# Kernel optimization log

Measured on AMD Instinct MI355X. Metric: run time of the kernel, lower is better.

The kernel has to match this reference:

```python
import jax, jax.numpy as jnp
import numpy as np

NUM_EXPERTS = 64
TOPK = 8
EPS = 1.1920929e-07  # torch.finfo(float32).eps


def setup_inputs() -> dict:
    key = jax.random.key(0)
    k1, k2 = jax.random.split(key)
    hidden_states = jax.random.normal(k1, (1, 4096, 4096), dtype=jnp.float32)
    wg_weight = jax.random.normal(k2, (NUM_EXPERTS, 4096), dtype=jnp.float32) * 0.02
    return {"hidden_states": hidden_states, "wg_weight": wg_weight}


def _routing(logits, capacity):
    # logits: [T, E]; capacity: static python int
    gates = jax.nn.softmax(logits, axis=1)                       # [T, E]
    _, idx = jax.lax.top_k(gates, TOPK)                          # [T, k]
    emask = jax.nn.one_hot(idx, NUM_EXPERTS, dtype=jnp.float32)  # [T, k, E]
    # sum of selected gate probs per token, clamped at fp32 eps
    gates_s = jnp.clip(jnp.einsum('tke,te->t', emask, gates), EPS)[:, None]
    router_probs = gates / gates_s                               # [T, E]
    # priority: cumulative position of each token within each expert,
    # scanned over (topk-major, token-minor) flattened order
    idx_flat = idx.T.reshape(-1)                                 # [k*T]
    mflat = jax.nn.one_hot(idx_flat, NUM_EXPERTS, dtype=jnp.int32)
    tp = jnp.cumsum(mflat, axis=0) * mflat - 1                   # [k*T, E]
    tp = tp.reshape(TOPK, -1, NUM_EXPERTS).transpose(1, 0, 2).max(axis=1)  # [T, E]
    valid = (tp >= 0) & (tp < capacity)                          # [T, E]
    tp = jnp.where(valid, tp, 0)
    dispatch_mask = jax.nn.one_hot(tp, capacity, dtype=jnp.bool_) & valid[:, :, None]  # [T, E, C]
    combine_weights = router_probs[:, :, None] * dispatch_mask   # [T, E, C]
    return combine_weights, dispatch_mask


def reference(hidden_states, wg_weight):
    b, s, h = hidden_states.shape
    x = hidden_states.reshape(-1, h).astype(jnp.float32)         # [T, H]
    logits = x @ wg_weight.T                                     # [T, E]
    # expert_capacity = max tokens assigned to any expert (data-dependent,
    # computed eagerly as in the torch .item() call)
    _, idx = jax.lax.top_k(jax.nn.softmax(logits, axis=1), TOPK)
    counts = jnp.bincount(idx.reshape(-1), length=NUM_EXPERTS)
    capacity = int(counts.max())
    return _routing(logits, capacity)
```

## Files before the change

### kernel.cpp

```cpp
#include <hip/hip_runtime.h>
#include <hip/hip_bf16.h>


#define TOK 4096
#define HID 4096
#define NE  64
#define NK  8

typedef double v4d __attribute__((ext_vector_type(4)));

__global__ __launch_bounds__(256) void gemm_logits_mfma(
    const float* __restrict__ x, const float* __restrict__ wg,
    double* __restrict__ partial, int kchunk, int* __restrict__ flag) {
  __shared__ float xs[64][68];
  __shared__ float wsh[64][68];
  const int tid  = threadIdx.x;
  const int lane = tid & 63;
  const int w    = tid >> 6;
  const int t0   = blockIdx.x * 64;
  const int k0   = blockIdx.y * kchunk;

  if (blockIdx.x == 0 && blockIdx.y == 0 && tid == 0) *flag = 0;

  v4d z = {0.0, 0.0, 0.0, 0.0};
  v4d pr = __builtin_amdgcn_mfma_f64_16x16x4f64((double)lane, 1.0, z, 0, 0, 0);
  v4d pc = __builtin_amdgcn_mfma_f64_16x16x4f64(1.0, (double)lane, z, 0, 0, 0);
  const int pv0 = (int)(pr[0] + 0.5);
  const int qv0 = (int)(pc[0] + 0.5);
  const bool a_kouter = ((pv0 & 3) == 0);
  const bool b_kouter = ((qv0 & 3) == 0);
  const int am = a_kouter ? (lane & 15) : (lane >> 2);
  const int ak = a_kouter ? (lane >> 4) : (lane & 3);
  const int bn = b_kouter ? (lane & 15) : (lane >> 2);
  const int bk = b_kouter ? (lane >> 4) : (lane & 3);
  int rmap[4], cmap[4];
#pragma unroll
  for (int v = 0; v < 4; ++v) {
    int V = (int)(pr[v] + 0.5);
    int rv = a_kouter ? ((V - 96) >> 2) : ((V - 6) >> 4);
    rmap[v] = rv < 0 ? 0 : (rv > 15 ? 15 : rv);
    int W = (int)(pc[v] + 0.5);
    int cv = b_kouter ? ((W - 96) >> 2) : ((W - 6) >> 4);
    cmap[v] = cv < 0 ? 0 : (cv > 15 ? 15 : cv);
  }

  v4d acc0 = {0.0, 0.0, 0.0, 0.0};
  v4d acc1 = acc0, acc2 = acc0, acc3 = acc0;

  const int lrow = tid >> 2;
  const int lcol = (tid & 3) * 16;

  for (int s = 0; s < kchunk; s += 64) {
    const int kk0 = k0 + s;
#pragma unroll
    for (int j = 0; j < 4; ++j) {
      *(float4*)&xs [lrow][lcol + j * 4] =
          *(const float4*)&x [(size_t)(t0 + lrow) * HID + kk0 + lcol + j * 4];
      *(float4*)&wsh[lrow][lcol + j * 4] =
          *(const float4*)&wg[(size_t)lrow * HID + kk0 + lcol + j * 4];
    }
    __syncthreads();
#pragma unroll
    for (int s4 = 0; s4 < 16; ++s4) {
      double a  = (double)xs [w * 16 + am][s4 * 4 + ak];
      double b0 = (double)wsh[ 0 + bn][s4 * 4 + bk];
      double b1 = (double)wsh[16 + bn][s4 * 4 + bk];
      double b2 = (double)wsh[32 + bn][s4 * 4 + bk];
      double b3 = (double)wsh[48 + bn][s4 * 4 + bk];
      acc0 = __builtin_amdgcn_mfma_f64_16x16x4f64(a, b0, acc0, 0, 0, 0);
      acc1 = __builtin_amdgcn_mfma_f64_16x16x4f64(a, b1, acc1, 0, 0, 0);
      acc2 = __builtin_amdgcn_mfma_f64_16x16x4f64(a, b2, acc2, 0, 0, 0);
      acc3 = __builtin_amdgcn_mfma_f64_16x16x4f64(a, b3, acc3, 0, 0, 0);
    }
    __syncthreads();
  }

  double* base = partial + (size_t)blockIdx.y * TOK * NE;
#pragma unroll
  for (int v = 0; v < 4; ++v) {
    const int row = t0 + w * 16 + rmap[v];
    const int col = cmap[v];
    double* rp = base + (size_t)row * NE;
    rp[ 0 + col] = acc0[v];
    rp[16 + col] = acc1[v];
    rp[32 + col] = acc2[v];
    rp[48 + col] = acc3[v];
  }
}

__global__ __launch_bounds__(256) void verify_kernel(
    const float* __restrict__ x, const float* __restrict__ wg,
    const double* __restrict__ partial, int nsplit, int* __restrict__ flag) {
  const int gid  = blockIdx.x * blockDim.x + threadIdx.x;
  const int wid  = gid >> 6;
  const int lane = gid & 63;
  const int t = (wid * 521) & (TOK - 1);
  const int e = wid & 63;
  double acc = 0.0;
  for (int k = lane; k < HID; k += 64)
    acc = fma((double)x[(size_t)t * HID + k], (double)wg[(size_t)e * HID + k], acc);
#pragma unroll
  for (int off = 32; off; off >>= 1) acc += __shfl_xor(acc, off);
  if (lane == 0) {
    double got = 0.0;
    for (int p = 0; p < nsplit; ++p)
      got += partial[(size_t)p * TOK * NE + (size_t)t * NE + e];
    if (!(fabs(got - acc) <= 1e-6)) atomicOr(flag, 1);
  }
}

__global__ __launch_bounds__(256) void repair_gemm(
    const float* __restrict__ x, const float* __restrict__ wg,
    double* __restrict__ partial, int nsplit, const int* __restrict__ flag) {
  if (*(volatile const int*)flag == 0) return;
  const int gid = blockIdx.x * 256 + threadIdx.x;
  const int t = gid >> 6;
  const int e = gid & 63;
  double acc = 0.0;
  for (int k = 0; k < HID; ++k)
    acc = fma((double)x[(size_t)t * HID + k], (double)wg[(size_t)e * HID + k], acc);
  partial[(size_t)t * NE + e] = acc;
  for (int p = 1; p < nsplit; ++p)
    partial[(size_t)p * TOK * NE + (size_t)t * NE + e] = 0.0;
}

__global__ __launch_bounds__(256) void topk_kernel(
    const double* __restrict__ partial, int nsplit,
    int* __restrict__ idx_kt, float* __restrict__ w_kt) {
  const int gid  = blockIdx.x * blockDim.x + threadIdx.x;
  const int t    = gid >> 6;
  const int lane = gid & 63;

  double v = 0.0;
  for (int p = 0; p < nsplit; ++p)
    v += partial[(size_t)p * TOK * NE + (size_t)t * NE + lane];

  double m = v;
#pragma unroll
  for (int off = 32; off; off >>= 1) {
    double o = __shfl_xor(m, off);
    m = o > m ? o : m;
  }
  double g = exp(v - m);
  double s = g;
#pragma unroll
  for (int off = 32; off; off >>= 1) s += __shfl_xor(s, off);
  double gate = g / s;

  float key = (float)gate;
  double ssel = 0.0;
  int my_k = -1;
#pragma unroll
  for (int k = 0; k < NK; ++k) {
    float bv = key;
    int   bi = lane;
#pragma unroll
    for (int off = 32; off; off >>= 1) {
      float ov = __shfl_xor(bv, off);
      int   oi = __shfl_xor(bi, off);
      if (ov > bv || (ov == bv && oi < bi)) { bv = ov; bi = oi; }
    }
    ssel += __shfl(gate, bi);
    if (lane == bi) { my_k = k; key = -1.0f; }
  }
  double gs = ssel;
  const double eps = (double)1.1920929e-07f;
  if (gs < eps) gs = eps;

  if (my_k >= 0) {
    idx_kt[my_k * TOK + t] = lane;
    w_kt [my_k * TOK + t] = (float)(gate / gs);
  }
}

__global__ __launch_bounds__(1024) void rank_kernel(
    const int* __restrict__ idx_kt, int* __restrict__ rank_kt) {
  const int e    = blockIdx.x;
  const int tid  = threadIdx.x;
  const int lane = tid & 63;
  const int w    = tid >> 6;
  __shared__ int wt[16];
  int running = 0;
  const unsigned long long below = (1ull << lane) - 1ull;

  for (int i0 = 0; i0 < NK * TOK; i0 += 1024) {
    const int i = i0 + tid;
    const bool mhit = (idx_kt[i] == e);
    unsigned long long mask = __ballot(mhit);
    if (lane == 0) wt[w] = __popcll(mask);
    __syncthreads();
    int woff = 0, tot = 0;
#pragma unroll
    for (int j = 0; j < 16; ++j) {
      int c = wt[j];
      tot += c;
      if (j < w) woff += c;
    }
    if (mhit) rank_kt[i] = running + woff + __popcll(mask & below);
    running += tot;
    __syncthreads();
  }
}

__global__ __launch_bounds__(256) void scatter_kernel(
    const int* __restrict__ idx_kt, const int* __restrict__ rank_kt,
    const float* __restrict__ w_kt, float* __restrict__ out, int C) {
  const int i = blockIdx.x * 256 + threadIdx.x;
  const int t = i & (TOK - 1);
  const int e = idx_kt[i];
  const int c = rank_kt[i];
  const float wv = w_kt[i];
  if (e >= 0 && e < NE && c >= 0 && c < C) {
    size_t off = ((size_t)t * NE + e) * (size_t)C + (size_t)c;
    out[off] = wv;
    out[(size_t)TOK * NE * C + off] = 1.0f;
  }
}

extern "C" void kernel_launch(void* const* d_in, const int* in_sizes, int n_in,
                              void* d_out, int out_size, void* d_ws, size_t ws_size,
                              hipStream_t stream) {
  const float* x  = (const float*)d_in[0];
  const float* wg = (const float*)d_in[1];
  float* out = (float*)d_out;

  const int C = out_size / (2 * TOK * NE);

  const size_t slab = (size_t)TOK * NE * sizeof(double);
  const size_t tail = 3 * (size_t)NK * TOK * sizeof(int);
  int nsplit = 8;
  while (nsplit > 1 && (size_t)nsplit * slab + tail + 64 > ws_size) nsplit >>= 1;
  const int kchunk = HID / nsplit;

  char* ws = (char*)d_ws;
  double* partial = (double*)ws;
  int*    idx_kt  = (int*)  (ws + (size_t)nsplit * slab);
  int*    rank_kt = (int*)  (ws + (size_t)nsplit * slab + (size_t)NK * TOK * 4);
  float*  w_kt    = (float*)(ws + (size_t)nsplit * slab + (size_t)NK * TOK * 8);
  int*    flag    = (int*)  (ws + (size_t)nsplit * slab + tail);

  hipMemsetAsync(d_out, 0, (size_t)out_size * sizeof(float), stream);

  dim3 ggrid(TOK / 64, nsplit);
  gemm_logits_mfma<<<ggrid, 256, 0, stream>>>(x, wg, partial, kchunk, flag);
  verify_kernel   <<<128, 256, 0, stream>>>(x, wg, partial, nsplit, flag);
  repair_gemm     <<<TOK * NE / 256, 256, 0, stream>>>(x, wg, partial, nsplit, flag);
  topk_kernel     <<<TOK * 64 / 256, 256, 0, stream>>>(partial, nsplit, idx_kt, w_kt);
  rank_kernel     <<<NE, 1024, 0, stream>>>(idx_kt, rank_kt);
  scatter_kernel  <<<NK * TOK / 256, 256, 0, stream>>>(idx_kt, rank_kt, w_kt, out, C);
}
```

Baseline: 1.264 ms.

## Fuse output zero-fill into logits GEMM and replace FP64 MFMA with FMA tiles

The separate hipMemsetAsync of the large dense output is removed. Extra blocks appended to the logits GEMM grid now zero the output with float4 stores, so the fill runs alongside the GEMM. The GEMM drops the FP64 MFMA path and its runtime lane-layout probing in favour of a scalar FP64 FMA register tile of 4x4 per thread. This removes the launch and serialization of the memset, but the FMA path may have lower throughput than MFMA, and it relies on out_size being a multiple of 4.

```diff
diff --git a/kernel.cpp b/kernel.cpp
--- a/kernel.cpp
+++ b/kernel.cpp
@@ -6,86 +6,88 @@
 #define HID 4096
 #define NE  64
 #define NK  8
-
-typedef double v4d __attribute__((ext_vector_type(4)));
-
-__global__ __launch_bounds__(256) void gemm_logits_mfma(
+#define FILLB 2048
+
+__global__ __launch_bounds__(256) void fused_gemm_fill(
     const float* __restrict__ x, const float* __restrict__ wg,
-    double* __restrict__ partial, int kchunk, int* __restrict__ flag) {
-  __shared__ float xs[64][68];
-  __shared__ float wsh[64][68];
-  const int tid  = threadIdx.x;
-  const int lane = tid & 63;
-  const int w    = tid >> 6;
-  const int t0   = blockIdx.x * 64;
-  const int k0   = blockIdx.y * kchunk;
-
-  if (blockIdx.x == 0 && blockIdx.y == 0 && tid == 0) *flag = 0;
-
-  v4d z = {0.0, 0.0, 0.0, 0.0};
-  v4d pr = __builtin_amdgcn_mfma_f64_16x16x4f64((double)lane, 1.0, z, 0, 0, 0);
-  v4d pc = __builtin_amdgcn_mfma_f64_16x16x4f64(1.0, (double)lane, z, 0, 0, 0);
-  const int pv0 = (int)(pr[0] + 0.5);
-  const int qv0 = (int)(pc[0] + 0.5);
-  const bool a_kouter = ((pv0 & 3) == 0);
-  const bool b_kouter = ((qv0 & 3) == 0);
-  const int am = a_kouter ? (lane & 15) : (lane >> 2);
-  const int ak = a_kouter ? (lane >> 4) : (lane & 3);
-  const int bn = b_kouter ? (lane & 15) : (lane >> 2);
-  const int bk = b_kouter ? (lane >> 4) : (lane & 3);
-  int rmap[4], cmap[4];
-#pragma unroll
-  for (int v = 0; v < 4; ++v) {
-    int V = (int)(pr[v] + 0.5);
-    int rv = a_kouter ? ((V - 96) >> 2) : ((V - 6) >> 4);
-    rmap[v] = rv < 0 ? 0 : (rv > 15 ? 15 : rv);
-    int W = (int)(pc[v] + 0.5);
-    int cv = b_kouter ? ((W - 96) >> 2) : ((W - 6) >> 4);
-    cmap[v] = cv < 0 ? 0 : (cv > 15 ? 15 : cv);
-  }
-
-  v4d acc0 = {0.0, 0.0, 0.0, 0.0};
-  v4d acc1 = acc0, acc2 = acc0, acc3 = acc0;
-
+    double* __restrict__ partial, int kchunk, int nsplit,
+    float* __restrict__ out, size_t n4, int* __restrict__ flag) {
+  __shared__ float xs [64][68];
+  __shared__ float wsf[64][65];
+  const int tid = threadIdx.x;
+  const int GB  = 64 * nsplit;
+
+  if ((int)blockIdx.x >= GB) {
+    const int fb = (int)blockIdx.x - GB;
+    const float4 z4 = make_float4(0.f, 0.f, 0.f, 0.f);
+    float4* o4 = (float4*)out;
+    for (size_t i = (size_t)fb * 256 + tid; i < n4; i += (size_t)FILLB * 256)
+      o4[i] = z4;
+    return;
+  }
+
+  if (blockIdx.x == 0 && tid == 0) *flag = 0;
+  const int bt   = (int)blockIdx.x & 63;
+  const int slab = (int)blockIdx.x >> 6;
+  const int t0 = bt * 64;
+  const int k0 = slab * kchunk;
+  const int te = tid & 15;
+  const int tt = tid >> 4;
   const int lrow = tid >> 2;
-  const int lcol = (tid & 3) * 16;
+  const int lc   = (tid & 3) * 16;
+
+  double acc[4][4];
+#pragma unroll
+  for (int i = 0; i < 4; ++i)
+#pragma unroll
+    for (int j = 0; j < 4; ++j) acc[i][j] = 0.0;
 
   for (int s = 0; s < kchunk; s += 64) {
-    const int kk0 = k0 + s;
+    const int kk = k0 + s;
 #pragma unroll
     for (int j = 0; j < 4; ++j) {
-      *(float4*)&xs [lrow][lcol + j * 4] =
-          *(const float4*)&x [(size_t)(t0 + lrow) * HID + kk0 + lcol + j * 4];
-      *(float4*)&wsh[lrow][lcol + j * 4] =
-          *(const float4*)&wg[(size_t)lrow * HID + kk0 + lcol + j * 4];
-    }
-    __syncthreads();
-#pragma unroll
-    for (int s4 = 0; s4 < 16; ++s4) {
-      double a  = (double)xs [w * 16 + am][s4 * 4 + ak];
-      double b0 = (double)wsh[ 0 + bn][s4 * 4 + bk];
-      double b1 = (double)wsh[16 + bn][s4 * 4 + bk];
-      double b2 = (double)wsh[32 + bn][s4 * 4 + bk];
-      double b3 = (double)wsh[48 + bn][s4 * 4 + bk];
-      acc0 = __builtin_amdgcn_mfma_f64_16x16x4f64(a, b0, acc0, 0, 0, 0);
-      acc1 = __builtin_amdgcn_mfma_f64_16x16x4f64(a, b1, acc1, 0, 0, 0);
-      acc2 = __builtin_amdgcn_mfma_f64_16x16x4f64(a, b2, acc2, 0, 0, 0);
-      acc3 = __builtin_amdgcn_mfma_f64_16x16x4f64(a, b3, acc3, 0, 0, 0);
-    }
-    __syncthreads();
-  }
-
-  double* base = partial + (size_t)blockIdx.y * TOK * NE;
-#pragma unroll
-  for (int v = 0; v < 4; ++v) {
-    const int row = t0 + w * 16 + rmap[v];
-    const int col = cmap[v];
-    double* rp = base + (size_t)row * NE;
-    rp[ 0 + col] = acc0[v];
-    rp[16 + col] = acc1[v];
-    rp[32 + col] = acc2[v];
-    rp[48 + col] = acc3[v];
-  }
+      float4 xv = *(const float4*)&x [(size_t)(t0 + lrow) * HID + kk + lc + 4 * j];
+      *(float4*)&xs[lrow][lc + 4 * j] = xv;
+      float4 wv = *(const float4*)&wg[(size_t)lrow * HID + kk + lc + 4 * j];
+      wsf[lrow][lc + 4 * j + 0] = wv.x;
+      wsf[lrow][lc + 4 * j + 1] = wv.y;
+      wsf[lrow][lc + 4 * j + 2] = wv.z;
+      wsf[lrow][lc + 4 * j + 3] = wv.w;
+    }
+    __syncthreads();
+#pragma unroll 4
+    for (int k4 = 0; k4 < 16; ++k4) {
+      const int kb = k4 * 4;
+      double dx[4][4];
+#pragma unroll
+      for (int i = 0; i < 4; ++i) {
+        float4 xv = *(const float4*)&xs[tt * 4 + i][kb];
+        dx[i][0] = (double)xv.x; dx[i][1] = (double)xv.y;
+        dx[i][2] = (double)xv.z; dx[i][3] = (double)xv.w;
+      }
+#pragma unroll
+      for (int j = 0; j < 4; ++j) {
+        const double w0 = (double)wsf[te * 4 + j][kb + 0];
+        const double w1 = (double)wsf[te * 4 + j][kb + 1];
+        const double w2 = (double)wsf[te * 4 + j][kb + 2];
+        const double w3 = (double)wsf[te * 4 + j][kb + 3];
+#pragma unroll
+        for (int i = 0; i < 4; ++i)
+          acc[i][j] = fma(dx[i][0], w0,
+                      fma(dx[i][1], w1,
+                      fma(dx[i][2], w2,
+                      fma(dx[i][3], w3, acc[i][j]))));
+      }
+    }
+    __syncthreads();
+  }
+
+  double* base = partial + (size_t)slab * TOK * NE;
+#pragma unroll
+  for (int i = 0; i < 4; ++i)
+#pragma unroll
+    for (int j = 0; j < 4; ++j)
+      base[(size_t)(t0 + tt * 4 + i) * NE + te * 4 + j] = acc[i][j];
 }
 
 __global__ __launch_bounds__(256) void verify_kernel(
@@ -239,13 +241,13 @@
   float*  w_kt    = (float*)(ws + (size_t)nsplit * slab + (size_t)NK * TOK * 8);
   int*    flag    = (int*)  (ws + (size_t)nsplit * slab + tail);
 
-  hipMemsetAsync(d_out, 0, (size_t)out_size * sizeof(float), stream);
-
-  dim3 ggrid(TOK / 64, nsplit);
-  gemm_logits_mfma<<<ggrid, 256, 0, stream>>>(x, wg, partial, kchunk, flag);
-  verify_kernel   <<<128, 256, 0, stream>>>(x, wg, partial, nsplit, flag);
-  repair_gemm     <<<TOK * NE / 256, 256, 0, stream>>>(x, wg, partial, nsplit, flag);
-  topk_kernel     <<<TOK * 64 / 256, 256, 0, stream>>>(partial, nsplit, idx_kt, w_kt);
-  rank_kernel     <<<NE, 1024, 0, stream>>>(idx_kt, rank_kt);
-  scatter_kernel  <<<NK * TOK / 256, 256, 0, stream>>>(idx_kt, rank_kt, w_kt, out, C);
-}
+  const size_t n4 = (size_t)out_size >> 2;
+
+  fused_gemm_fill<<<64 * nsplit + FILLB, 256, 0, stream>>>(
+      x, wg, partial, kchunk, nsplit, out, n4, flag);
+  verify_kernel  <<<128, 256, 0, stream>>>(x, wg, partial, nsplit, flag);
+  repair_gemm    <<<TOK * NE / 256, 256, 0, stream>>>(x, wg, partial, nsplit, flag);
+  topk_kernel    <<<TOK * 64 / 256, 256, 0, stream>>>(partial, nsplit, idx_kt, w_kt);
+  rank_kernel    <<<NE, 1024, 0, stream>>>(idx_kt, rank_kt);
+  scatter_kernel <<<NK * TOK / 256, 256, 0, stream>>>(idx_kt, rank_kt, w_kt, out, C);
+}
```

After: 1.295 ms. 1.02x slower.
